# Kernel optimization log

Hardware: AMD Instinct MI355X
Metric: run time of the kernel (lower is better)

The kernel has to match this reference:

```python
import jax, jax.numpy as jnp
import numpy as np

B, N, S, HID, HEADS = 64, 256, 16, 32, 8
BN_EPS = 1e-5


def setup_inputs() -> dict:
    key = jax.random.key(0)
    k1, k2, k3, k4 = jax.random.split(key, 4)
    stacks = jax.random.normal(k1, (B, N, N, S), dtype=jnp.float32)
    # True = padded node (row masked out), like the torch code's `mask`
    mask = jax.random.bernoulli(k2, 0.2, (B, N))
    # BatchNorm1d(S) params (train mode -> batch stats; affine params below)
    gamma = jnp.ones((S,), jnp.float32)
    beta = jnp.zeros((S,), jnp.float32)
    # Linear(S -> HID), ReLU, Linear(HID -> HEADS)
    W1 = jax.random.normal(k3, (S, HID), dtype=jnp.float32) * (1.0 / np.sqrt(S))
    b1 = jnp.zeros((HID,), jnp.float32)
    W2 = jax.random.normal(k4, (HID, HEADS), dtype=jnp.float32) * (1.0 / np.sqrt(HID))
    b2 = jnp.zeros((HEADS,), jnp.float32)
    return {"stacks": stacks, "mask": mask, "gamma": gamma, "beta": beta,
            "W1": W1, "b1": b1, "W2": W2, "b2": b2}


def reference(stacks, mask, gamma, beta, W1, b1, W2, b2):
    # stacks: [b, n, n, S]; mask: [b, n] bool, True = padded.
    # Torch: rows stacks[~mask] (shape [K, n, S]) are flattened to [K*n, S],
    # passed through BN(train) + Linear + ReLU + Linear, and scattered back
    # into a zero [b, n, n, heads] tensor. Equivalent dense formulation:
    # compute BN stats as a masked mean/var over valid rows, apply the MLP
    # everywhere, then zero out masked rows.
    valid = ~mask                                   # [b, n]
    w = valid.astype(stacks.dtype)[:, :, None, None]  # [b, n, 1, 1]
    n1 = stacks.shape[2]
    count = jnp.sum(valid.astype(stacks.dtype)) * n1  # K * n valid BN rows
    sx = jnp.sum(stacks * w, axis=(0, 1, 2))        # [S]
    sx2 = jnp.sum((stacks * stacks) * w, axis=(0, 1, 2))
    mean = sx / count
    var = sx2 / count - mean * mean                 # biased var (BN train mode)
    xn = (stacks - mean) * (gamma / jnp.sqrt(var + BN_EPS)) + beta
    h = jax.nn.relu(jnp.einsum('bnms,sh->bnmh', xn, W1) + b1)
    y = jnp.einsum('bnmh,hk->bnmk', h, W2) + b2     # [b, n, n, heads]
    return jnp.where(valid[:, :, None, None], y, jnp.zeros((), y.dtype))
```

## Files before the change

kernel.cpp:

```cpp
#include <hip/hip_runtime.h>
#include <hip/hip_bf16.h>

#define BB 64
#define NN 256
#define SS 16
#define HH 32
#define KK 8
#define NROWPAIRS (BB*NN)
#define STATS_BLOCKS 2048


__global__ void prep_kernel(const void* __restrict__ mask_raw,
                            int* __restrict__ mode_out,
                            int* __restrict__ count_out,
                            unsigned char* __restrict__ valid,
                            float* __restrict__ sx,
                            float* __restrict__ sx2) {
    int tid = threadIdx.x;
    if (tid < 16) { sx[tid] = 0.0f; sx2[tid] = 0.0f; }

    __shared__ int s_flags[2];
    __shared__ int s_mode;
    __shared__ int s_count;
    if (tid < 2) s_flags[tid] = 0;
    if (tid == 0) s_count = 0;
    __syncthreads();

    const unsigned int* w = (const unsigned int*)mask_raw;
    int f_float = 0, f_bool = 0;
    for (int i = tid; i < 4096; i += 1024) {
        unsigned int v = w[i];
        if (v == 0x3F800000u) f_float = 1;
        if (((v >> 8) & 0xFFu) == 1u || ((v >> 16) & 0xFFu) == 1u ||
            ((v >> 24) & 0xFFu) == 1u) f_bool = 1;
    }
    if (f_float) atomicOr(&s_flags[0], 1);
    if (f_bool)  atomicOr(&s_flags[1], 1);
    __syncthreads();
    if (tid == 0) {
        int mode = s_flags[1] ? 1 : (s_flags[0] ? 2 : 0);
        s_mode = mode;
        *mode_out = mode;
    }
    __syncthreads();
    int mode = s_mode;

    int localc = 0;
    for (int i = tid; i < NROWPAIRS; i += 1024) {
        int masked;
        if (mode == 1)      masked = ((const unsigned char*)mask_raw)[i] != 0;
        else if (mode == 2) masked = ((const float*)mask_raw)[i] != 0.0f;
        else                masked = ((const int*)mask_raw)[i] != 0;
        unsigned char v = (unsigned char)(masked ? 0 : 1);
        valid[i] = v;
        localc += v;
    }
    atomicAdd(&s_count, localc);
    __syncthreads();
    if (tid == 0) *count_out = s_count;
}

__global__ __launch_bounds__(256) void stats_kernel(
        const float* __restrict__ stacks,
        const unsigned char* __restrict__ valid,
        float* __restrict__ sx, float* __restrict__ sx2) {
    int tid = threadIdx.x;
    float4 s1 = make_float4(0.f, 0.f, 0.f, 0.f);
    float4 s2 = make_float4(0.f, 0.f, 0.f, 0.f);

    for (int k = 0; k < NROWPAIRS / STATS_BLOCKS; ++k) {
        int chunk = blockIdx.x + k * STATS_BLOCKS;
        if (!valid[chunk]) continue;
        const float4* p = (const float4*)stacks + (size_t)chunk * 1024;
        #pragma unroll
        for (int it = 0; it < 4; ++it) {
            float4 v = p[tid + it * 256];
            s1.x += v.x; s1.y += v.y; s1.z += v.z; s1.w += v.w;
            s2.x += v.x * v.x; s2.y += v.y * v.y;
            s2.z += v.z * v.z; s2.w += v.w * v.w;
        }
    }

    __shared__ float lds[8 * 256];
    lds[0 * 256 + tid] = s1.x; lds[1 * 256 + tid] = s1.y;
    lds[2 * 256 + tid] = s1.z; lds[3 * 256 + tid] = s1.w;
    lds[4 * 256 + tid] = s2.x; lds[5 * 256 + tid] = s2.y;
    lds[6 * 256 + tid] = s2.z; lds[7 * 256 + tid] = s2.w;
    __syncthreads();

    if (tid < 32) {
        int kind = tid >> 4;
        int s = tid & 15;
        int g = s >> 2, c = (s & 3) + kind * 4;
        float tot = 0.f;
        for (int i = 0; i < 64; ++i) tot += lds[c * 256 + (g + i * 4)];
        atomicAdd(kind ? &sx2[s] : &sx[s], tot);
    }
}

__global__ void weights_kernel(const float* __restrict__ gamma,
                               const float* __restrict__ beta,
                               const float* __restrict__ W1,
                               const float* __restrict__ b1,
                               const float* __restrict__ sx,
                               const float* __restrict__ sx2,
                               const int* __restrict__ count_rows,
                               float* __restrict__ W1c,
                               float* __restrict__ b1c) {
    __shared__ float s_scale[SS], s_shift[SS];
    int tid = threadIdx.x;
    if (tid < SS) {
        float cnt = (float)(*count_rows) * (float)NN;
        if (cnt < 1.0f) cnt = 1.0f;
        float mean = sx[tid] / cnt;
        float var  = sx2[tid] / cnt - mean * mean;
        float sc   = gamma[tid] / sqrtf(var + 1e-5f);
        s_scale[tid] = sc;
        s_shift[tid] = beta[tid] - mean * sc;
    }
    __syncthreads();
    if (tid < SS * HH) W1c[tid] = s_scale[tid >> 5] * W1[tid];
    if (tid < HH) {
        float acc = b1[tid];
        #pragma unroll
        for (int s = 0; s < SS; ++s) acc += s_shift[s] * W1[s * HH + tid];
        b1c[tid] = acc;
    }
}

__global__ __launch_bounds__(256) void mlp_kernel(
        const float* __restrict__ stacks,
        const unsigned char* __restrict__ valid,
        const float* __restrict__ W1c,
        const float* __restrict__ b1c,
        const float* __restrict__ W2,
        const float* __restrict__ b2,
        float* __restrict__ out) {
    int bid = blockIdx.x;
    int tid = threadIdx.x;
    size_t row = (size_t)bid * NN + tid;
    float4* outp = (float4*)out + row * 2;

    if (!valid[bid]) {
        float4 z = make_float4(0.f, 0.f, 0.f, 0.f);
        outp[0] = z; outp[1] = z;
        return;
    }

    const float4* xp = (const float4*)stacks + row * 4;
    float4 x0 = xp[0], x1 = xp[1], x2 = xp[2], x3 = xp[3];
    float x[SS] = { x0.x, x0.y, x0.z, x0.w,  x1.x, x1.y, x1.z, x1.w,
                    x2.x, x2.y, x2.z, x2.w,  x3.x, x3.y, x3.z, x3.w };

    float h[HH];
    #pragma unroll
    for (int j = 0; j < HH; ++j) h[j] = b1c[j];
    #pragma unroll
    for (int k = 0; k < SS; ++k) {
        float xk = x[k];
        #pragma unroll
        for (int j = 0; j < HH; ++j) h[j] = fmaf(xk, W1c[k * HH + j], h[j]);
    }
    #pragma unroll
    for (int j = 0; j < HH; ++j) h[j] = fmaxf(h[j], 0.0f);

    float y[KK];
    #pragma unroll
    for (int i = 0; i < KK; ++i) y[i] = b2[i];
    #pragma unroll
    for (int j = 0; j < HH; ++j) {
        float hj = h[j];
        #pragma unroll
        for (int i = 0; i < KK; ++i) y[i] = fmaf(hj, W2[j * KK + i], y[i]);
    }

    outp[0] = make_float4(y[0], y[1], y[2], y[3]);
    outp[1] = make_float4(y[4], y[5], y[6], y[7]);
}

extern "C" void kernel_launch(void* const* d_in, const int* in_sizes, int n_in,
                              void* d_out, int out_size, void* d_ws, size_t ws_size,
                              hipStream_t stream) {
    const float* stacks = (const float*)d_in[0];
    const void*  mask   = d_in[1];
    const float* gamma  = (const float*)d_in[2];
    const float* beta   = (const float*)d_in[3];
    const float* W1     = (const float*)d_in[4];
    const float* b1     = (const float*)d_in[5];
    const float* W2     = (const float*)d_in[6];
    const float* b2     = (const float*)d_in[7];
    float* out = (float*)d_out;

    char* ws = (char*)d_ws;
    int*           mode      = (int*)(ws + 0);
    int*           countRows = (int*)(ws + 4);
    unsigned char* valid     = (unsigned char*)(ws + 64);
    float*         sx        = (float*)(ws + 16448);
    float*         sx2       = (float*)(ws + 16512);
    float*         b1c       = (float*)(ws + 16576);
    float*         W1c       = (float*)(ws + 16704);

    prep_kernel<<<1, 1024, 0, stream>>>(mask, mode, countRows, valid, sx, sx2);
    stats_kernel<<<STATS_BLOCKS, 256, 0, stream>>>(stacks, valid, sx, sx2);
    weights_kernel<<<1, 512, 0, stream>>>(gamma, beta, W1, b1, sx, sx2,
                                          countRows, W1c, b1c);
    mlp_kernel<<<NROWPAIRS, 256, 0, stream>>>(stacks, valid, W1c, b1c, W2, b2, out);
}
```

Baseline: 482.8 us.

## Stage MLP input rows through LDS with 64-thread blocks, four rows per thread

The MLP kernel now uses one 64-thread wavefront per row pair. The wave loads the 256x16 input tile into shared memory with coalesced float4 loads, transposed so the data is laid out by feature. Each thread then computes four output rows, splitting the hidden layer into two halves of 16 to limit register pressure. The point is to reuse each weight load across four rows and to coalesce the global reads. The costs are an LDS transpose, a barrier, more registers per thread and fewer threads per block.

```diff
diff --git a/kernel.cpp b/kernel.cpp
--- a/kernel.cpp
+++ b/kernel.cpp
@@ -128,7 +128,7 @@
     }
 }
 
-__global__ __launch_bounds__(256) void mlp_kernel(
+__global__ __launch_bounds__(64) void mlp_kernel(
         const float* __restrict__ stacks,
         const unsigned char* __restrict__ valid,
         const float* __restrict__ W1c,
@@ -137,45 +137,98 @@
         const float* __restrict__ b2,
         float* __restrict__ out) {
     int bid = blockIdx.x;
-    int tid = threadIdx.x;
-    size_t row = (size_t)bid * NN + tid;
-    float4* outp = (float4*)out + row * 2;
+    int t = threadIdx.x;
+    float4* outp = (float4*)out + (size_t)bid * 512;
 
     if (!valid[bid]) {
         float4 z = make_float4(0.f, 0.f, 0.f, 0.f);
-        outp[0] = z; outp[1] = z;
+        #pragma unroll
+        for (int it = 0; it < 8; ++it) outp[it * 64 + t] = z;
         return;
     }
 
-    const float4* xp = (const float4*)stacks + row * 4;
-    float4 x0 = xp[0], x1 = xp[1], x2 = xp[2], x3 = xp[3];
-    float x[SS] = { x0.x, x0.y, x0.z, x0.w,  x1.x, x1.y, x1.z, x1.w,
-                    x2.x, x2.y, x2.z, x2.w,  x3.x, x3.y, x3.z, x3.w };
-
-    float h[HH];
-    #pragma unroll
-    for (int j = 0; j < HH; ++j) h[j] = b1c[j];
-    #pragma unroll
-    for (int k = 0; k < SS; ++k) {
-        float xk = x[k];
-        #pragma unroll
-        for (int j = 0; j < HH; ++j) h[j] = fmaf(xk, W1c[k * HH + j], h[j]);
-    }
-    #pragma unroll
-    for (int j = 0; j < HH; ++j) h[j] = fmaxf(h[j], 0.0f);
-
-    float y[KK];
-    #pragma unroll
-    for (int i = 0; i < KK; ++i) y[i] = b2[i];
-    #pragma unroll
-    for (int j = 0; j < HH; ++j) {
-        float hj = h[j];
-        #pragma unroll
-        for (int i = 0; i < KK; ++i) y[i] = fmaf(hj, W2[j * KK + i], y[i]);
-    }
-
-    outp[0] = make_float4(y[0], y[1], y[2], y[3]);
-    outp[1] = make_float4(y[4], y[5], y[6], y[7]);
+    __shared__ float xs[SS * 256];
+    const float4* xp = (const float4*)stacks + (size_t)bid * 1024;
+    #pragma unroll
+    for (int it = 0; it < 16; ++it) {
+        float4 v = xp[it * 64 + t];
+        int row = it * 16 + (t >> 2);
+        int c0 = (t & 3) * 4;
+        xs[(c0 + 0) * 256 + row] = v.x;
+        xs[(c0 + 1) * 256 + row] = v.y;
+        xs[(c0 + 2) * 256 + row] = v.z;
+        xs[(c0 + 3) * 256 + row] = v.w;
+    }
+    __syncthreads();
+
+    float4 b2v0 = ((const float4*)b2)[0];
+    float4 b2v1 = ((const float4*)b2)[1];
+    float y[4][8];
+    #pragma unroll
+    for (int r = 0; r < 4; ++r) {
+        y[r][0] = b2v0.x; y[r][1] = b2v0.y; y[r][2] = b2v0.z; y[r][3] = b2v0.w;
+        y[r][4] = b2v1.x; y[r][5] = b2v1.y; y[r][6] = b2v1.z; y[r][7] = b2v1.w;
+    }
+
+    #pragma unroll
+    for (int half = 0; half < 2; ++half) {
+        float hb[16];
+        {
+            const float4* bp = (const float4*)b1c + half * 4;
+            #pragma unroll
+            for (int q = 0; q < 4; ++q) {
+                float4 v = bp[q];
+                hb[q * 4 + 0] = v.x; hb[q * 4 + 1] = v.y;
+                hb[q * 4 + 2] = v.z; hb[q * 4 + 3] = v.w;
+            }
+        }
+        float h[4][16];
+        #pragma unroll
+        for (int r = 0; r < 4; ++r)
+            #pragma unroll
+            for (int j = 0; j < 16; ++j) h[r][j] = hb[j];
+
+        #pragma unroll
+        for (int k = 0; k < 16; ++k) {
+            float wk[16];
+            const float4* wp = (const float4*)W1c + k * 8 + half * 4;
+            #pragma unroll
+            for (int q = 0; q < 4; ++q) {
+                float4 v = wp[q];
+                wk[q * 4 + 0] = v.x; wk[q * 4 + 1] = v.y;
+                wk[q * 4 + 2] = v.z; wk[q * 4 + 3] = v.w;
+            }
+            float xk[4];
+            #pragma unroll
+            for (int r = 0; r < 4; ++r) xk[r] = xs[k * 256 + t + 64 * r];
+            #pragma unroll
+            for (int r = 0; r < 4; ++r)
+                #pragma unroll
+                for (int j = 0; j < 16; ++j)
+                    h[r][j] = fmaf(xk[r], wk[j], h[r][j]);
+        }
+
+        #pragma unroll
+        for (int j = 0; j < 16; ++j) {
+            const float4* w2p = (const float4*)W2 + (half * 16 + j) * 2;
+            float4 a = w2p[0], b = w2p[1];
+            float w2r[8] = {a.x, a.y, a.z, a.w, b.x, b.y, b.z, b.w};
+            #pragma unroll
+            for (int r = 0; r < 4; ++r) {
+                float hr = fmaxf(h[r][j], 0.0f);
+                #pragma unroll
+                for (int i = 0; i < 8; ++i)
+                    y[r][i] = fmaf(hr, w2r[i], y[r][i]);
+            }
+        }
+    }
+
+    #pragma unroll
+    for (int r = 0; r < 4; ++r) {
+        int row = t + 64 * r;
+        outp[row * 2 + 0] = make_float4(y[r][0], y[r][1], y[r][2], y[r][3]);
+        outp[row * 2 + 1] = make_float4(y[r][4], y[r][5], y[r][6], y[r][7]);
+    }
 }
 
 extern "C" void kernel_launch(void* const* d_in, const int* in_sizes, int n_in,
@@ -204,5 +257,5 @@
     stats_kernel<<<STATS_BLOCKS, 256, 0, stream>>>(stacks, valid, sx, sx2);
     weights_kernel<<<1, 512, 0, stream>>>(gamma, beta, W1, b1, sx, sx2,
                                           countRows, W1c, b1c);
-    mlp_kernel<<<NROWPAIRS, 256, 0, stream>>>(stacks, valid, W1c, b1c, W2, b2, out);
-}
+    mlp_kernel<<<NROWPAIRS, 64, 0, stream>>>(stacks, valid, W1c, b1c, W2, b2, out);
+}
```

Measured after the change: 503.3 us. 1.04x slower.
